# Optimization experiments

Hardware: AMD Instinct MI355X
Metric: run time of the kernel (lower is better)

The kernel has to match this reference:

```python
import jax, jax.numpy as jnp
import numpy as np

NB_VARS = 2_000_000
N0 = 2 + 2 * NB_VARS      # input vector length: [zero, one, pos0, neg0, pos1, neg1, ...]
M0 = 4_000_000            # prod layer 0 outputs (binary fan-in)
M1 = 1_000_000            # sum  layer 1 outputs (irregular fan-in)
M2 = 500_000              # prod layer 2 outputs (binary fan-in)
M3 = 125_000              # sum  layer 3 outputs (irregular fan-in)


def setup_inputs() -> dict:
    key = jax.random.key(0)
    ks = jax.random.split(key, 7)
    x_pos = jax.random.uniform(ks[0], (NB_VARS,), dtype=jnp.float32)
    ix_in0 = jax.random.randint(ks[1], (2 * M0,), 0, N0)            # edges of prod layer 0
    ix_in1 = jax.random.randint(ks[2], (8_000_000,), 0, M0)         # edges of sum layer 1
    ix_out1 = jnp.sort(jax.random.randint(ks[3], (8_000_000,), 0, M1))
    ix_in2 = jax.random.randint(ks[4], (2 * M2,), 0, M1)            # edges of prod layer 2
    ix_in3 = jax.random.randint(ks[5], (1_000_000,), 0, M2)         # edges of sum layer 3
    ix_out3 = jnp.sort(jax.random.randint(ks[6], (1_000_000,), 0, M3))
    return {"x_pos": x_pos, "ix_in0": ix_in0, "ix_in1": ix_in1, "ix_out1": ix_out1,
            "ix_in2": ix_in2, "ix_in3": ix_in3, "ix_out3": ix_out3}


def reference(x_pos, ix_in0, ix_in1, ix_out1, ix_in2, ix_in3, ix_out3):
    # encode_input (real semiring): neg = negate(pos) = 1 - pos; interleave; prepend [zero=0, one=1]
    neg = 1.0 - x_pos
    units = jnp.array([0.0, 1.0], dtype=x_pos.dtype)
    x = jnp.concatenate([units, jnp.stack([x_pos, neg], axis=1).reshape(-1)])  # [N0]

    # layer 0: product layer, binary fan-in -> gather + pairwise multiply
    e0 = x[ix_in0].reshape(M0, 2)
    x = e0[:, 0] * e0[:, 1]                                                    # [M0]

    # layer 1: sum layer, irregular fan-in -> gather + segment-sum
    x = jax.ops.segment_sum(x[ix_in1], ix_out1, num_segments=M1)               # [M1]

    # layer 2: product layer, binary fan-in
    e2 = x[ix_in2].reshape(M2, 2)
    x = e2[:, 0] * e2[:, 1]                                                    # [M2]

    # layer 3: sum layer, irregular fan-in
    x = jax.ops.segment_sum(x[ix_in3], ix_out3, num_segments=M3)               # [M3]
    return x
```

## Files before the change

### kernel.cpp

```cpp
#include <hip/hip_runtime.h>
#include <hip/hip_bf16.h>


#define WIN_BITS 20
#define PERS_BLOCKS 2048
#define PERS_THREADS 256

template<int NS, int NWIN>
__global__ __launch_bounds__(PERS_THREADS)
void sum_win_kernel(const float* __restrict__ vin,
                    const int4* __restrict__ ix_in4,
                    const int4* __restrict__ ix_out4,
                    float* __restrict__ out, int nT4) {
    const int nTh  = gridDim.x * blockDim.x;
    const int gtid = blockIdx.x * blockDim.x + threadIdx.x;
    const int lane = threadIdx.x & 63;

    int4  a[NS];
    float4 v[NS];
    bool  act[NS];
    #pragma unroll
    for (int s = 0; s < NS; ++s) {
        int t = s * nTh + gtid;
        act[s] = (t < nT4);
        a[s] = act[s] ? ix_in4[t] : make_int4(-1, -1, -1, -1);
        v[s] = make_float4(0.f, 0.f, 0.f, 0.f);
    }

    #pragma unroll
    for (int w = 0; w < NWIN; ++w) {
        #pragma unroll
        for (int s = 0; s < NS; ++s) {
            if ((a[s].x >> WIN_BITS) == w) v[s].x = vin[a[s].x];
            if ((a[s].y >> WIN_BITS) == w) v[s].y = vin[a[s].y];
            if ((a[s].z >> WIN_BITS) == w) v[s].z = vin[a[s].z];
            if ((a[s].w >> WIN_BITS) == w) v[s].w = vin[a[s].w];
        }
    }

    #pragma unroll
    for (int s = 0; s < NS; ++s) {
        int t = s * nTh + gtid;
        int4 sg = act[s] ? ix_out4[t] : make_int4(-1, -1, -1, -1);
        int seg = -1; float val = 0.f;
        if (act[s]) {
            int cur = sg.x; float acc = v[s].x;
            if (sg.y == cur) acc += v[s].y; else { atomicAdd(&out[cur], acc); cur = sg.y; acc = v[s].y; }
            if (sg.z == cur) acc += v[s].z; else { atomicAdd(&out[cur], acc); cur = sg.z; acc = v[s].z; }
            if (sg.w == cur) acc += v[s].w; else { atomicAdd(&out[cur], acc); cur = sg.w; acc = v[s].w; }
            seg = cur; val = acc;
        }
        #pragma unroll
        for (int off = 1; off < 64; off <<= 1) {
            float vv = __shfl_up(val, off, 64);
            int   ss = __shfl_up(seg, off, 64);
            if (lane >= off && ss == seg) val += vv;
        }
        int seg_next = __shfl_down(seg, 1, 64);
        bool is_last = (lane == 63) || (seg_next != seg);
        if (act[s] && is_last) atomicAdd(&out[seg], val);
    }
}

__device__ __forceinline__ void mul_factor(const float* __restrict__ xp,
                                           int idx, int w, float& acc) {
    if (idx < 2) {
        if (w == 0) acc *= (float)idx;
    } else {
        int k = (idx - 2) >> 1;
        if ((k >> WIN_BITS) == w) {
            float v = xp[k];
            acc *= (idx & 1) ? 1.0f - v : v;
        }
    }
}

template<int NS, int NWIN>
__global__ __launch_bounds__(PERS_THREADS)
void prod_win_kernel(const float* __restrict__ x_pos,
                     const int4* __restrict__ ix,
                     float4* __restrict__ out, int nT) {
    const int nTh  = gridDim.x * blockDim.x;
    const int gtid = blockIdx.x * blockDim.x + threadIdx.x;

    int4 p0[NS], p1[NS];
    bool act[NS];
    float a0[NS], a1[NS], a2[NS], a3[NS];
    #pragma unroll
    for (int s = 0; s < NS; ++s) {
        int t = s * nTh + gtid;
        act[s] = (t < nT);
        p0[s] = act[s] ? ix[2 * t]     : make_int4(0, 0, 0, 0);
        p1[s] = act[s] ? ix[2 * t + 1] : make_int4(0, 0, 0, 0);
        a0[s] = 1.f; a1[s] = 1.f; a2[s] = 1.f; a3[s] = 1.f;
    }

    #pragma unroll
    for (int w = 0; w < NWIN; ++w) {
        #pragma unroll
        for (int s = 0; s < NS; ++s) {
            mul_factor(x_pos, p0[s].x, w, a0[s]); mul_factor(x_pos, p0[s].y, w, a0[s]);
            mul_factor(x_pos, p0[s].z, w, a1[s]); mul_factor(x_pos, p0[s].w, w, a1[s]);
            mul_factor(x_pos, p1[s].x, w, a2[s]); mul_factor(x_pos, p1[s].y, w, a2[s]);
            mul_factor(x_pos, p1[s].z, w, a3[s]); mul_factor(x_pos, p1[s].w, w, a3[s]);
        }
    }

    #pragma unroll
    for (int s = 0; s < NS; ++s) {
        if (act[s]) {
            int t = s * nTh + gtid;
            float4 r; r.x = a0[s]; r.y = a1[s]; r.z = a2[s]; r.w = a3[s];
            out[t] = r;
        }
    }
}

__global__ void prod2_kernel(const float* __restrict__ vin,
                             const int4* __restrict__ ix,
                             float2* __restrict__ out, int nT) {
    int t = blockIdx.x * blockDim.x + threadIdx.x;
    if (t >= nT) return;
    int4 p = ix[t];
    float a0 = vin[p.x], b0 = vin[p.y];
    float a1 = vin[p.z], b1 = vin[p.w];
    float2 r; r.x = a0 * b0; r.y = a1 * b1;
    out[t] = r;
}

extern "C" void kernel_launch(void* const* d_in, const int* in_sizes, int n_in,
                              void* d_out, int out_size, void* d_ws, size_t ws_size,
                              hipStream_t stream) {
    const float* x_pos  = (const float*)d_in[0];
    const int*   ix_in0 = (const int*)d_in[1];
    const int*   ix_in1 = (const int*)d_in[2];
    const int*   ix_out1= (const int*)d_in[3];
    const int*   ix_in2 = (const int*)d_in[4];
    const int*   ix_in3 = (const int*)d_in[5];
    const int*   ix_out3= (const int*)d_in[6];
    float* out = (float*)d_out;

    const int M0 = in_sizes[1] / 2;
    const int E1 = in_sizes[2];
    const int M1 = 1000000;
    const int M2 = in_sizes[4] / 2;
    const int E3 = in_sizes[5];
    const int M3 = out_size;

    float* y0 = (float*)d_ws;
    float* y1 = y0 + M0;
    float* y2 = y1 + M1;

    hipMemsetAsync(y1,  0, (size_t)M1 * sizeof(float), stream);
    hipMemsetAsync(out, 0, (size_t)M3 * sizeof(float), stream);

    int t0 = M0 / 4;
    prod_win_kernel<2, 2><<<PERS_BLOCKS, PERS_THREADS, 0, stream>>>(
        x_pos, (const int4*)ix_in0, (float4*)y0, t0);

    int t1 = E1 / 4;
    sum_win_kernel<4, 4><<<PERS_BLOCKS, PERS_THREADS, 0, stream>>>(
        y0, (const int4*)ix_in1, (const int4*)ix_out1, y1, t1);

    int t2 = M2 / 2;
    prod2_kernel<<<(t2 + 255) / 256, 256, 0, stream>>>(
        y1, (const int4*)ix_in2, (float2*)y2, t2);

    int t3 = E3 / 4;
    sum_win_kernel<1, 1><<<(t3 + PERS_THREADS - 1) / PERS_THREADS, PERS_THREADS, 0, stream>>>(
        y2, (const int4*)ix_in3, (const int4*)ix_out3, out, t3);
}
```

Baseline: 295.3 us.

## Store layer-0 inputs and outputs in fp16 to shrink gather footprint

```diff
diff --git a/kernel.cpp b/kernel.cpp
--- a/kernel.cpp
+++ b/kernel.cpp
@@ -1,24 +1,67 @@
 #include <hip/hip_runtime.h>
-#include <hip/hip_bf16.h>
+#include <hip/hip_fp16.h>
 
 
-#define WIN_BITS 20
 #define PERS_BLOCKS 2048
 #define PERS_THREADS 256
+#define WBITS_F32 20
+#define WBITS_F16 21
+
+__global__ void cvt16_kernel(const float4* __restrict__ in,
+                             uint2* __restrict__ out, int n4) {
+    int t = blockIdx.x * blockDim.x + threadIdx.x;
+    if (t >= n4) return;
+    float4 f = in[t];
+    __half2 lo = __floats2half2_rn(f.x, f.y);
+    __half2 hi = __floats2half2_rn(f.z, f.w);
+    uint2 r;
+    r.x = *(const unsigned int*)&lo;
+    r.y = *(const unsigned int*)&hi;
+    out[t] = r;
+}
+
+__device__ __forceinline__ float decode16(const __half* __restrict__ xp, int idx) {
+    int k = (idx - 2) >> 1;
+    k = k < 0 ? 0 : k;
+    float v = __half2float(xp[k]);
+    v = (idx & 1) ? 1.0f - v : v;
+    if (idx < 2) v = (float)idx;
+    return v;
+}
+
+__global__ void layer0_prod4_kernel(const __half* __restrict__ x16,
+                                    const int4* __restrict__ ix,
+                                    uint2* __restrict__ out16,
+                                    int nT) {
+    int t = blockIdx.x * blockDim.x + threadIdx.x;
+    if (t >= nT) return;
+    int4 p0 = ix[2 * t];
+    int4 p1 = ix[2 * t + 1];
+    float a0 = decode16(x16, p0.x), b0 = decode16(x16, p0.y);
+    float a1 = decode16(x16, p0.z), b1 = decode16(x16, p0.w);
+    float a2 = decode16(x16, p1.x), b2 = decode16(x16, p1.y);
+    float a3 = decode16(x16, p1.z), b3 = decode16(x16, p1.w);
+    __half2 lo = __floats2half2_rn(a0 * b0, a1 * b1);
+    __half2 hi = __floats2half2_rn(a2 * b2, a3 * b3);
+    uint2 r;
+    r.x = *(const unsigned int*)&lo;
+    r.y = *(const unsigned int*)&hi;
+    out16[t] = r;
+}
 
 template<int NS, int NWIN>
 __global__ __launch_bounds__(PERS_THREADS)
-void sum_win_kernel(const float* __restrict__ vin,
-                    const int4* __restrict__ ix_in4,
-                    const int4* __restrict__ ix_out4,
-                    float* __restrict__ out, int nT4) {
+void sum_win_h_kernel(const __half* __restrict__ vin,
+                      const int4* __restrict__ ix_in4,
+                      const int4* __restrict__ ix_out4,
+                      float* __restrict__ out, int nT4) {
     const int nTh  = gridDim.x * blockDim.x;
     const int gtid = blockIdx.x * blockDim.x + threadIdx.x;
     const int lane = threadIdx.x & 63;
 
-    int4  a[NS];
+    int4   a[NS];
     float4 v[NS];
-    bool  act[NS];
+    bool   act[NS];
     #pragma unroll
     for (int s = 0; s < NS; ++s) {
         int t = s * nTh + gtid;
@@ -31,10 +74,10 @@
     for (int w = 0; w < NWIN; ++w) {
         #pragma unroll
         for (int s = 0; s < NS; ++s) {
-            if ((a[s].x >> WIN_BITS) == w) v[s].x = vin[a[s].x];
-            if ((a[s].y >> WIN_BITS) == w) v[s].y = vin[a[s].y];
-            if ((a[s].z >> WIN_BITS) == w) v[s].z = vin[a[s].z];
-            if ((a[s].w >> WIN_BITS) == w) v[s].w = vin[a[s].w];
+            if ((a[s].x >> WBITS_F16) == w) v[s].x = __half2float(vin[a[s].x]);
+            if ((a[s].y >> WBITS_F16) == w) v[s].y = __half2float(vin[a[s].y]);
+            if ((a[s].z >> WBITS_F16) == w) v[s].z = __half2float(vin[a[s].z]);
+            if ((a[s].w >> WBITS_F16) == w) v[s].w = __half2float(vin[a[s].w]);
         }
     }
 
@@ -62,58 +105,32 @@
     }
 }
 
-__device__ __forceinline__ void mul_factor(const float* __restrict__ xp,
-                                           int idx, int w, float& acc) {
-    if (idx < 2) {
-        if (w == 0) acc *= (float)idx;
-    } else {
-        int k = (idx - 2) >> 1;
-        if ((k >> WIN_BITS) == w) {
-            float v = xp[k];
-            acc *= (idx & 1) ? 1.0f - v : v;
-        }
+__global__ void sum4_f32_kernel(const float* __restrict__ vin,
+                                const int4* __restrict__ ix_in4,
+                                const int4* __restrict__ ix_out4,
+                                float* __restrict__ out, int nT4) {
+    int t = blockIdx.x * blockDim.x + threadIdx.x;
+    int lane = threadIdx.x & 63;
+    int seg = -1; float val = 0.f;
+    if (t < nT4) {
+        int4 a  = ix_in4[t];
+        int4 sg = ix_out4[t];
+        float v0 = vin[a.x], v1 = vin[a.y], v2 = vin[a.z], v3 = vin[a.w];
+        int cur = sg.x; float acc = v0;
+        if (sg.y == cur) acc += v1; else { atomicAdd(&out[cur], acc); cur = sg.y; acc = v1; }
+        if (sg.z == cur) acc += v2; else { atomicAdd(&out[cur], acc); cur = sg.z; acc = v2; }
+        if (sg.w == cur) acc += v3; else { atomicAdd(&out[cur], acc); cur = sg.w; acc = v3; }
+        seg = cur; val = acc;
     }
-}
-
-template<int NS, int NWIN>
-__global__ __launch_bounds__(PERS_THREADS)
-void prod_win_kernel(const float* __restrict__ x_pos,
-                     const int4* __restrict__ ix,
-                     float4* __restrict__ out, int nT) {
-    const int nTh  = gridDim.x * blockDim.x;
-    const int gtid = blockIdx.x * blockDim.x + threadIdx.x;
-
-    int4 p0[NS], p1[NS];
-    bool act[NS];
-    float a0[NS], a1[NS], a2[NS], a3[NS];
     #pragma unroll
-    for (int s = 0; s < NS; ++s) {
-        int t = s * nTh + gtid;
-        act[s] = (t < nT);
-        p0[s] = act[s] ? ix[2 * t]     : make_int4(0, 0, 0, 0);
-        p1[s] = act[s] ? ix[2 * t + 1] : make_int4(0, 0, 0, 0);
-        a0[s] = 1.f; a1[s] = 1.f; a2[s] = 1.f; a3[s] = 1.f;
+    for (int off = 1; off < 64; off <<= 1) {
+        float vv = __shfl_up(val, off, 64);
+        int   ss = __shfl_up(seg, off, 64);
+        if (lane >= off && ss == seg) val += vv;
     }
-
-    #pragma unroll
-    for (int w = 0; w < NWIN; ++w) {
-        #pragma unroll
-        for (int s = 0; s < NS; ++s) {
-            mul_factor(x_pos, p0[s].x, w, a0[s]); mul_factor(x_pos, p0[s].y, w, a0[s]);
-            mul_factor(x_pos, p0[s].z, w, a1[s]); mul_factor(x_pos, p0[s].w, w, a1[s]);
-            mul_factor(x_pos, p1[s].x, w, a2[s]); mul_factor(x_pos, p1[s].y, w, a2[s]);
-            mul_factor(x_pos, p1[s].z, w, a3[s]); mul_factor(x_pos, p1[s].w, w, a3[s]);
-        }
-    }
-
-    #pragma unroll
-    for (int s = 0; s < NS; ++s) {
-        if (act[s]) {
-            int t = s * nTh + gtid;
-            float4 r; r.x = a0[s]; r.y = a1[s]; r.z = a2[s]; r.w = a3[s];
-            out[t] = r;
-        }
-    }
+    int seg_next = __shfl_down(seg, 1, 64);
+    bool is_last = (lane == 63) || (seg_next != seg);
+    if (t < nT4 && is_last) atomicAdd(&out[seg], val);
 }
 
 __global__ void prod2_kernel(const float* __restrict__ vin,
@@ -140,6 +157,7 @@
     const int*   ix_out3= (const int*)d_in[6];
     float* out = (float*)d_out;
 
+    const int NV = in_sizes[0];
     const int M0 = in_sizes[1] / 2;
     const int E1 = in_sizes[2];
     const int M1 = 1000000;
@@ -147,26 +165,34 @@
     const int E3 = in_sizes[5];
     const int M3 = out_size;
 
-    float* y0 = (float*)d_ws;
-    float* y1 = y0 + M0;
-    float* y2 = y1 + M1;
+    char* ws = (char*)d_ws;
+    __half* y0  = (__half*)(ws);
+    float*  y1  = (float*)(ws + (size_t)8  * 1024 * 1024);
+    float*  y2  = (float*)(ws + (size_t)12 * 1024 * 1024);
+    __half* x16 = (__half*)(ws + (size_t)14 * 1024 * 1024);
 
     hipMemsetAsync(y1,  0, (size_t)M1 * sizeof(float), stream);
     hipMemsetAsync(out, 0, (size_t)M3 * sizeof(float), stream);
 
+    const int B = 256;
+
+    int nc = NV / 4;
+    cvt16_kernel<<<(nc + B - 1) / B, B, 0, stream>>>(
+        (const float4*)x_pos, (uint2*)x16, nc);
+
     int t0 = M0 / 4;
-    prod_win_kernel<2, 2><<<PERS_BLOCKS, PERS_THREADS, 0, stream>>>(
-        x_pos, (const int4*)ix_in0, (float4*)y0, t0);
+    layer0_prod4_kernel<<<(t0 + B - 1) / B, B, 0, stream>>>(
+        x16, (const int4*)ix_in0, (uint2*)y0, t0);
 
     int t1 = E1 / 4;
-    sum_win_kernel<4, 4><<<PERS_BLOCKS, PERS_THREADS, 0, stream>>>(
+    sum_win_h_kernel<4, 2><<<PERS_BLOCKS, PERS_THREADS, 0, stream>>>(
         y0, (const int4*)ix_in1, (const int4*)ix_out1, y1, t1);
 
     int t2 = M2 / 2;
-    prod2_kernel<<<(t2 + 255) / 256, 256, 0, stream>>>(
+    prod2_kernel<<<(t2 + B - 1) / B, B, 0, stream>>>(
         y1, (const int4*)ix_in2, (float2*)y2, t2);
 
     int t3 = E3 / 4;
-    sum_win_kernel<1, 1><<<(t3 + PERS_THREADS - 1) / PERS_THREADS, PERS_THREADS, 0, stream>>>(
+    sum4_f32_kernel<<<(t3 + B - 1) / B, B, 0, stream>>>(
         y2, (const int4*)ix_in3, (const int4*)ix_out3, out, t3);
 }
```

After: 252.9 us. -14.4%, faster.
